# Performance work log

Hardware: AMD Instinct MI355X
Metric: run time of the kernel (lower is better)

The kernel has to match this reference:

```python
import jax, jax.numpy as jnp
import numpy as np

B, S, D, H = 2, 2048, 1024, 16
HD = D // H
SCALE_FACTOR = 0.2  # ScalableSoftmax scale


def setup_inputs() -> dict:
    key = jax.random.key(0)
    ks = jax.random.split(key, 5)
    inv = 1.0 / np.sqrt(D)
    return {
        "x": jax.random.normal(ks[0], (B, S, D), dtype=jnp.float32),
        "qkv_w": jax.random.normal(ks[1], (3 * D, D), dtype=jnp.float32) * inv,
        "qkv_b": jax.random.normal(ks[2], (3 * D,), dtype=jnp.float32) * 0.02,
        "out_w": jax.random.normal(ks[3], (D, D), dtype=jnp.float32) * inv,
        "out_b": jax.random.normal(ks[4], (D,), dtype=jnp.float32) * 0.02,
    }


def reference(x, qkv_w, qkv_b, out_w, out_b):
    b, s, d = x.shape
    # qkv projection: [b, s, 3d] -> [b, h, s, 3*hd]
    qkv = (jnp.einsum("bsd,ed->bse", x, qkv_w) + qkv_b)
    qkv = qkv.reshape(b, s, H, 3 * HD).transpose(0, 2, 1, 3)
    q, k, v = jnp.split(qkv, 3, axis=-1)  # each [b, h, s, hd]
    # scaled dot-product scores, then ScalableSoftmax: softmax(0.2 * scores)
    scores = jnp.einsum("bhqd,bhkd->bhqk", q, k) / jnp.sqrt(jnp.float32(HD))
    attn = jax.nn.softmax(SCALE_FACTOR * scores, axis=-1)
    vals = jnp.einsum("bhqk,bhkd->bhqd", attn, v)
    vals = vals.transpose(0, 2, 1, 3).reshape(b, s, d)
    return jnp.einsum("bsd,ed->bse", vals, out_w) + out_b
```

## Files before the change

### kernel.cpp

```cpp
#include <hip/hip_runtime.h>

using bh8    = __attribute__((ext_vector_type(8)))  short;
using f32x4v = __attribute__((ext_vector_type(4)))  float;
using f32x16 = __attribute__((ext_vector_type(16))) float;
using u32x4  = __attribute__((ext_vector_type(4)))  unsigned int;
using us4    = __attribute__((ext_vector_type(4)))  unsigned short;

#define AS1 __attribute__((address_space(1)))
#define AS3 __attribute__((address_space(3)))

#define B_  2
#define S_  2048
#define D_  1024
#define H_  16
#define HD_ 64
#define C2A 0.0360673760222241f

__device__ __forceinline__ unsigned short f2bf(float f) {
  unsigned u = __builtin_bit_cast(unsigned, f);
  return (unsigned short)((u + 0x7fffu + ((u >> 16) & 1u)) >> 16);
}
__device__ __forceinline__ int swz8(int r) { return (r ^ (r >> 3)) & 7; }

__global__ __launch_bounds__(256) void cvt_all(const float* __restrict__ x,
                                               const float* __restrict__ qw,
                                               const float* __restrict__ ow,
                                               unsigned short* __restrict__ xb,
                                               unsigned short* __restrict__ qwb,
                                               unsigned short* __restrict__ owb) {
  int i = blockIdx.x * 256 + threadIdx.x;
  const float* src; unsigned short* dst; int off;
  if (i < 1048576)      { src = x;  dst = xb;  off = i; }
  else if (i < 1835008) { src = qw; dst = qwb; off = i - 1048576; }
  else                  { src = ow; dst = owb; off = i - 1835008; }
  f32x4v v = reinterpret_cast<const f32x4v*>(src)[off];
  us4 o;
  o[0] = f2bf(v[0]); o[1] = f2bf(v[1]); o[2] = f2bf(v[2]); o[3] = f2bf(v[3]);
  reinterpret_cast<us4*>(dst)[off] = o;
}

template <int MODE, int BM>
__global__ __launch_bounds__(256) void gemm_bt(const unsigned short* __restrict__ A,
                                               const unsigned short* __restrict__ Bw,
                                               const float* __restrict__ bias,
                                               float* __restrict__ Cf,
                                               unsigned short* __restrict__ Qo,
                                               unsigned short* __restrict__ Ko,
                                               unsigned short* __restrict__ Vo,
                                               int M, int N, int K) {
  constexpr int NIW = (BM == 128) ? 4 : 2;
  constexpr int NA  = BM / 32;
  __shared__ __align__(16) short As[BM * 64];
  __shared__ __align__(16) short Bs[128 * 64];
  const int tid = threadIdx.x;
  const int w = tid >> 6, l = tid & 63;
  const int lr = l & 15, lg = l >> 4;
  const int m0 = blockIdx.x * BM, n0 = blockIdx.y * 128;
  const int wm = (BM == 128) ? (w >> 1) * 64 : 0;
  const int wn = (BM == 128) ? (w & 1) * 64 : w * 32;

  f32x4v acc[4][NIW];
#pragma unroll
  for (int a = 0; a < 4; a++)
#pragma unroll
    for (int b = 0; b < NIW; b++)
#pragma unroll
      for (int r = 0; r < 4; r++) acc[a][b][r] = 0.f;

#pragma unroll 1
  for (int k0 = 0; k0 < K; k0 += 64) {
    __syncthreads();
#pragma unroll
    for (int n = 0; n < NA; n++) {
      int idx = n * 256 + tid;
      int row = idx >> 3, p = idx & 7;
      int c = p ^ swz8(row);
      const unsigned short* srcA = A + (size_t)(m0 + row) * K + k0 + c * 8;
      __builtin_amdgcn_global_load_lds((const AS1 void*)srcA,
          (AS3 void*)((char*)As + (n * 256 + w * 64) * 16), 16, 0, 0);
    }
#pragma unroll
    for (int n = 0; n < 4; n++) {
      int idx = n * 256 + tid;
      int row = idx >> 3, p = idx & 7;
      int c = p ^ swz8(row);
      const unsigned short* srcB = Bw + (size_t)(n0 + row) * K + k0 + c * 8;
      __builtin_amdgcn_global_load_lds((const AS1 void*)srcB,
          (AS3 void*)((char*)Bs + (n * 256 + w * 64) * 16), 16, 0, 0);
    }
    __syncthreads();
#pragma unroll
    for (int kk = 0; kk < 2; kk++) {
      bh8 af[4], bf[NIW];
#pragma unroll
      for (int mi = 0; mi < 4; mi++) {
        int row = wm + mi * 16 + lr;
        int slot = (4 * kk + lg) ^ swz8(row);
        af[mi] = *(const bh8*)((const char*)As + row * 128 + slot * 16);
      }
#pragma unroll
      for (int ni = 0; ni < NIW; ni++) {
        int row = wn + ni * 16 + lr;
        int slot = (4 * kk + lg) ^ swz8(row);
        bf[ni] = *(const bh8*)((const char*)Bs + row * 128 + slot * 16);
      }
#pragma unroll
      for (int mi = 0; mi < 4; mi++)
#pragma unroll
        for (int ni = 0; ni < NIW; ni++)
          acc[mi][ni] = __builtin_amdgcn_mfma_f32_16x16x32_bf16(af[mi], bf[ni], acc[mi][ni], 0, 0, 0);
    }
  }

  if (MODE == 1) {
#pragma unroll
    for (int ni = 0; ni < NIW; ni++) {
      int e = n0 + wn + ni * 16 + lr;
      float bv = bias[e];
#pragma unroll
      for (int mi = 0; mi < 4; mi++) {
        int mbase = m0 + wm + mi * 16 + lg * 4;
#pragma unroll
        for (int r = 0; r < 4; r++)
          Cf[(size_t)(mbase + r) * N + e] = acc[mi][ni][r] + bv;
      }
    }
  } else {
#pragma unroll
    for (int ni = 0; ni < NIW; ni++) {
      int e = n0 + wn + ni * 16 + lr;
      int hh = e / 192;
      int rr = e - hh * 192;
      int tsel = rr >> 6, d = rr & 63;
      float bv = bias[e];
#pragma unroll
      for (int mi = 0; mi < 4; mi++) {
        int mbase = m0 + wm + mi * 16 + lg * 4;
#pragma unroll
        for (int r = 0; r < 4; r++) {
          int m = mbase + r;
          int b = m >> 11, s = m & 2047;
          float val = acc[mi][ni][r] + bv;
          size_t bh = (size_t)(b * H_ + hh);
          if (tsel == 0)      Qo[(bh * S_ + s) * HD_ + d] = f2bf(val * C2A);
          else if (tsel == 1) Ko[(bh * S_ + s) * HD_ + d] = f2bf(val);
          else                Vo[(bh * HD_ + d) * S_ + s] = f2bf(val);
        }
      }
    }
  }
}

__global__ __launch_bounds__(512) void attn_fwd(const unsigned short* __restrict__ Qt,
                                                const unsigned short* __restrict__ Kt,
                                                const unsigned short* __restrict__ VT,
                                                unsigned short* __restrict__ vals) {
  __shared__ __align__(16) short Ks[2 * 64 * 64];
  __shared__ __align__(16) short Vs[2 * 64 * 64];
  const int tid = threadIdx.x, w = tid >> 6, l = tid & 63;
  const int lq = l & 31, h = l >> 5;
  const int lin = blockIdx.x;
  const int uu_ = lin >> 3;
  const int bh = (lin & 7) + 8 * (uu_ & 3);
  const int q0 = (uu_ >> 2) * 256 + w * 32;
  const unsigned short* Qp = Qt + (size_t)bh * (S_ * HD_);
  const unsigned short* Kp = Kt + (size_t)bh * (S_ * HD_);
  const unsigned short* Vp = VT + (size_t)bh * (HD_ * S_);

  bh8 qf[4];
#pragma unroll
  for (int kf = 0; kf < 4; kf++)
    qf[kf] = *(const bh8*)(Qp + (size_t)(q0 + lq) * HD_ + kf * 16 + h * 8);

  f32x16 KZ;
#pragma unroll
  for (int r = 0; r < 16; r++) KZ[r] = 0.f;
  bh8 ones;
#pragma unroll
  for (int j = 0; j < 8; j++) ones[j] = (short)0x3F80;

  f32x16 O[2], Ol;
  O[0] = KZ; O[1] = KZ; Ol = KZ;

  const int row0 = tid >> 3, cc = (tid & 7) ^ swz8(row0);
  const unsigned short* kp0 = Kp + row0 * HD_ + cc * 8;
  const unsigned short* vp0 = Vp + (size_t)row0 * S_ + cc * 8;
  char* dK = (char*)Ks + w * 1024;
  char* dV = (char*)Vs + w * 1024;

  auto stage = [&](int t, int buf) {
    __builtin_amdgcn_global_load_lds((const AS1 void*)(kp0 + (size_t)t * 4096),
                                     (AS3 void*)(dK + buf * 8192), 16, 0, 0);
    __builtin_amdgcn_global_load_lds((const AS1 void*)(vp0 + (size_t)t * 64),
                                     (AS3 void*)(dV + buf * 8192), 16, 0, 0);
  };

  int ko0[4], ko1[4], vo0[4], vo1[4];
#pragma unroll
  for (int kf = 0; kf < 4; kf++) {
    int r0 = lq, r1 = 32 + lq;
    ko0[kf] = r0 * 128 + (((2 * kf + h) ^ swz8(r0)) << 4);
    ko1[kf] = r1 * 128 + (((2 * kf + h) ^ swz8(r1)) << 4);
  }
#pragma unroll
  for (int c = 0; c < 2; c++)
#pragma unroll
    for (int ni = 0; ni < 2; ni++) {
      int d = ni * 32 + lq;
      vo0[c * 2 + ni] = d * 128 + (((2 * c + h) ^ swz8(d)) << 4);
      vo1[c * 2 + ni] = d * 128 + (((4 + 2 * c + h) ^ swz8(d)) << 4);
    }

  stage(0, 0);
#pragma unroll 1
  for (int i = 0; i < 32; i++) {
    const int cur = i & 1;
    asm volatile("s_waitcnt vmcnt(0)" ::: "memory");
    __builtin_amdgcn_s_barrier();
    if (i < 31) stage(i + 1, cur ^ 1);
    const char* Kc = (const char*)Ks + cur * 8192;
    const char* Vc = (const char*)Vs + cur * 8192;

    f32x16 sa, sb;
    __builtin_amdgcn_s_setprio(1);
    {
      bh8 k0 = *(const bh8*)(Kc + ko0[0]);
      bh8 k1 = *(const bh8*)(Kc + ko1[0]);
      sa = __builtin_amdgcn_mfma_f32_32x32x16_bf16(k0, qf[0], KZ, 0, 0, 0);
      sb = __builtin_amdgcn_mfma_f32_32x32x16_bf16(k1, qf[0], KZ, 0, 0, 0);
    }
#pragma unroll
    for (int kf = 1; kf < 4; kf++) {
      bh8 k0 = *(const bh8*)(Kc + ko0[kf]);
      bh8 k1 = *(const bh8*)(Kc + ko1[kf]);
      sa = __builtin_amdgcn_mfma_f32_32x32x16_bf16(k0, qf[kf], sa, 0, 0, 0);
      sb = __builtin_amdgcn_mfma_f32_32x32x16_bf16(k1, qf[kf], sb, 0, 0, 0);
    }
    __builtin_amdgcn_s_setprio(0);

    float pa_[16], pb_[16];
#pragma unroll
    for (int r = 0; r < 16; r++)
      asm("v_exp_f32 %0, %1" : "=v"(pa_[r]) : "v"(sa[r]));
    unsigned wa0[4], wa1[4];
#pragma unroll
    for (int g = 0; g < 4; g++) {
      asm("v_cvt_pk_bf16_f32 %0, %1, %2" : "=v"(wa0[g]) : "v"(pa_[4 * g]), "v"(pa_[4 * g + 1]));
      asm("v_cvt_pk_bf16_f32 %0, %1, %2" : "=v"(wa1[g]) : "v"(pa_[4 * g + 2]), "v"(pa_[4 * g + 3]));
    }
#pragma unroll
    for (int r = 0; r < 16; r++)
      asm("v_exp_f32 %0, %1" : "=v"(pb_[r]) : "v"(sb[r]));
    unsigned wb0[4], wb1[4];
#pragma unroll
    for (int g = 0; g < 4; g++) {
      asm("v_cvt_pk_bf16_f32 %0, %1, %2" : "=v"(wb0[g]) : "v"(pb_[4 * g]), "v"(pb_[4 * g + 1]));
      asm("v_cvt_pk_bf16_f32 %0, %1, %2" : "=v"(wb1[g]) : "v"(pb_[4 * g + 2]), "v"(pb_[4 * g + 3]));
    }

    bh8 paf[2], pbf[2];
#pragma unroll
    for (int c = 0; c < 2; c++) {
      unsigned x0 = wa0[2 * c], y0 = wa0[2 * c + 1];
      unsigned x1 = wa1[2 * c], y1 = wa1[2 * c + 1];
      asm("v_permlane32_swap_b32 %0, %1" : "+v"(x0), "+v"(y0));
      asm("v_permlane32_swap_b32 %0, %1" : "+v"(x1), "+v"(y1));
      u32x4 up; up[0] = x0; up[1] = x1; up[2] = y0; up[3] = y1;
      paf[c] = __builtin_bit_cast(bh8, up);
    }
#pragma unroll
    for (int c = 0; c < 2; c++) {
      unsigned x0 = wb0[2 * c], y0 = wb0[2 * c + 1];
      unsigned x1 = wb1[2 * c], y1 = wb1[2 * c + 1];
      asm("v_permlane32_swap_b32 %0, %1" : "+v"(x0), "+v"(y0));
      asm("v_permlane32_swap_b32 %0, %1" : "+v"(x1), "+v"(y1));
      u32x4 up; up[0] = x0; up[1] = x1; up[2] = y0; up[3] = y1;
      pbf[c] = __builtin_bit_cast(bh8, up);
    }

    __builtin_amdgcn_s_setprio(1);
#pragma unroll
    for (int c = 0; c < 2; c++) {
      bh8 vf0 = *(const bh8*)(Vc + vo0[c * 2 + 0]);
      bh8 vf1 = *(const bh8*)(Vc + vo0[c * 2 + 1]);
      O[0] = __builtin_amdgcn_mfma_f32_32x32x16_bf16(paf[c], vf0, O[0], 0, 0, 0);
      O[1] = __builtin_amdgcn_mfma_f32_32x32x16_bf16(paf[c], vf1, O[1], 0, 0, 0);
      Ol   = __builtin_amdgcn_mfma_f32_32x32x16_bf16(paf[c], ones, Ol, 0, 0, 0);
    }
#pragma unroll
    for (int c = 0; c < 2; c++) {
      bh8 vf0 = *(const bh8*)(Vc + vo1[c * 2 + 0]);
      bh8 vf1 = *(const bh8*)(Vc + vo1[c * 2 + 1]);
      O[0] = __builtin_amdgcn_mfma_f32_32x32x16_bf16(pbf[c], vf0, O[0], 0, 0, 0);
      O[1] = __builtin_amdgcn_mfma_f32_32x32x16_bf16(pbf[c], vf1, O[1], 0, 0, 0);
      Ol   = __builtin_amdgcn_mfma_f32_32x32x16_bf16(pbf[c], ones, Ol, 0, 0, 0);
    }
    __builtin_amdgcn_s_setprio(0);
  }

  float rl[16];
#pragma unroll
  for (int r = 0; r < 16; r++) rl[r] = __builtin_amdgcn_rcpf(Ol[r]);

  const int b = bh >> 4, hh = bh & 15;
#pragma unroll
  for (int ni = 0; ni < 2; ni++) {
    int d = ni * 32 + lq;
#pragma unroll
    for (int r = 0; r < 16; r++) {
      float vvv = O[ni][r] * rl[r];
      int qg = q0 + 4 * h + 8 * (r >> 2) + (r & 3);
      vals[((size_t)(b * S_ + qg)) * D_ + hh * HD_ + d] = f2bf(vvv);
    }
  }
}

extern "C" void kernel_launch(void* const* d_in, const int* in_sizes, int n_in,
                              void* d_out, int out_size, void* d_ws, size_t ws_size,
                              hipStream_t stream) {
  const float* x     = (const float*)d_in[0];
  const float* qkv_w = (const float*)d_in[1];
  const float* qkv_b = (const float*)d_in[2];
  const float* out_w = (const float*)d_in[3];
  const float* out_b = (const float*)d_in[4];
  float* out = (float*)d_out;

  unsigned short* xb  = (unsigned short*)d_ws;
  unsigned short* qwb = xb  + (size_t)4096 * 1024;
  unsigned short* owb = qwb + (size_t)3072 * 1024;
  unsigned short* Qb  = owb + (size_t)1024 * 1024;
  unsigned short* Kb  = Qb  + (size_t)32 * 2048 * 64;
  unsigned short* Vb  = Kb  + (size_t)32 * 2048 * 64;
  unsigned short* vb  = Vb  + (size_t)32 * 2048 * 64;

  cvt_all<<<8192, 256, 0, stream>>>(x, qkv_w, out_w, xb, qwb, owb);
  gemm_bt<0, 128><<<dim3(32, 24), 256, 0, stream>>>(xb, qwb, qkv_b, nullptr, Qb, Kb, Vb,
                                                    4096, 3072, 1024);
  attn_fwd<<<256, 512, 0, stream>>>(Qb, Kb, Vb, vb);
  gemm_bt<1, 64><<<dim3(64, 8), 256, 0, stream>>>(vb, owb, out_b, out, nullptr, nullptr, nullptr,
                                                  4096, 1024, 1024);
}
```

Measured before the change: 116.9 us.

## Stage two KV tiles per barrier in attention and swizzle GEMM block order

The attention kernel now loads two 64-key K/V tiles per pipeline stage into doubled LDS buffers. This halves the number of barriers and vmcnt waits across the key loop and processes two tiles between each sync. Both GEMMs also remap block IDs so consecutive blocks are spread across the 8 XCDs for better L2 locality. The cost is more LDS per attention block (64KB) and a deeper unrolled body.

```diff
diff --git a/kernel.cpp b/kernel.cpp
--- a/kernel.cpp
+++ b/kernel.cpp
@@ -39,7 +39,7 @@
   reinterpret_cast<us4*>(dst)[off] = o;
 }
 
-template <int MODE, int BM>
+template <int MODE, int BM, int GX, int NW>
 __global__ __launch_bounds__(256) void gemm_bt(const unsigned short* __restrict__ A,
                                                const unsigned short* __restrict__ Bw,
                                                const float* __restrict__ bias,
@@ -55,7 +55,9 @@
   const int tid = threadIdx.x;
   const int w = tid >> 6, l = tid & 63;
   const int lr = l & 15, lg = l >> 4;
-  const int m0 = blockIdx.x * BM, n0 = blockIdx.y * 128;
+  const int lin = blockIdx.y * GX + blockIdx.x;
+  const int sw  = (lin & 7) * (NW / 8) + (lin >> 3);
+  const int m0 = (sw % GX) * BM, n0 = (sw / GX) * 128;
   const int wm = (BM == 128) ? (w >> 1) * 64 : 0;
   const int wn = (BM == 128) ? (w & 1) * 64 : w * 32;
 
@@ -155,8 +157,8 @@
                                                 const unsigned short* __restrict__ Kt,
                                                 const unsigned short* __restrict__ VT,
                                                 unsigned short* __restrict__ vals) {
-  __shared__ __align__(16) short Ks[2 * 64 * 64];
-  __shared__ __align__(16) short Vs[2 * 64 * 64];
+  __shared__ __align__(16) short Ks[2 * 2 * 64 * 64];
+  __shared__ __align__(16) short Vs[2 * 2 * 64 * 64];
   const int tid = threadIdx.x, w = tid >> 6, l = tid & 63;
   const int lq = l & 31, h = l >> 5;
   const int lin = blockIdx.x;
@@ -188,11 +190,17 @@
   char* dK = (char*)Ks + w * 1024;
   char* dV = (char*)Vs + w * 1024;
 
-  auto stage = [&](int t, int buf) {
-    __builtin_amdgcn_global_load_lds((const AS1 void*)(kp0 + (size_t)t * 4096),
-                                     (AS3 void*)(dK + buf * 8192), 16, 0, 0);
-    __builtin_amdgcn_global_load_lds((const AS1 void*)(vp0 + (size_t)t * 64),
-                                     (AS3 void*)(dV + buf * 8192), 16, 0, 0);
+  auto stage = [&](int i, int buf) {
+    const unsigned short* kB = kp0 + (size_t)i * 8192;
+    const unsigned short* vB = vp0 + (size_t)i * 128;
+    __builtin_amdgcn_global_load_lds((const AS1 void*)kB,
+                                     (AS3 void*)(dK + buf * 16384), 16, 0, 0);
+    __builtin_amdgcn_global_load_lds((const AS1 void*)(kB + 4096),
+                                     (AS3 void*)(dK + buf * 16384 + 8192), 16, 0, 0);
+    __builtin_amdgcn_global_load_lds((const AS1 void*)vB,
+                                     (AS3 void*)(dV + buf * 16384), 16, 0, 0);
+    __builtin_amdgcn_global_load_lds((const AS1 void*)(vB + 64),
+                                     (AS3 void*)(dV + buf * 16384 + 8192), 16, 0, 0);
   };
 
   int ko0[4], ko1[4], vo0[4], vo1[4];
@@ -213,89 +221,92 @@
 
   stage(0, 0);
 #pragma unroll 1
-  for (int i = 0; i < 32; i++) {
+  for (int i = 0; i < 16; i++) {
     const int cur = i & 1;
     asm volatile("s_waitcnt vmcnt(0)" ::: "memory");
     __builtin_amdgcn_s_barrier();
-    if (i < 31) stage(i + 1, cur ^ 1);
-    const char* Kc = (const char*)Ks + cur * 8192;
-    const char* Vc = (const char*)Vs + cur * 8192;
-
-    f32x16 sa, sb;
-    __builtin_amdgcn_s_setprio(1);
-    {
-      bh8 k0 = *(const bh8*)(Kc + ko0[0]);
-      bh8 k1 = *(const bh8*)(Kc + ko1[0]);
-      sa = __builtin_amdgcn_mfma_f32_32x32x16_bf16(k0, qf[0], KZ, 0, 0, 0);
-      sb = __builtin_amdgcn_mfma_f32_32x32x16_bf16(k1, qf[0], KZ, 0, 0, 0);
-    }
-#pragma unroll
-    for (int kf = 1; kf < 4; kf++) {
-      bh8 k0 = *(const bh8*)(Kc + ko0[kf]);
-      bh8 k1 = *(const bh8*)(Kc + ko1[kf]);
-      sa = __builtin_amdgcn_mfma_f32_32x32x16_bf16(k0, qf[kf], sa, 0, 0, 0);
-      sb = __builtin_amdgcn_mfma_f32_32x32x16_bf16(k1, qf[kf], sb, 0, 0, 0);
-    }
-    __builtin_amdgcn_s_setprio(0);
-
-    float pa_[16], pb_[16];
-#pragma unroll
-    for (int r = 0; r < 16; r++)
-      asm("v_exp_f32 %0, %1" : "=v"(pa_[r]) : "v"(sa[r]));
-    unsigned wa0[4], wa1[4];
-#pragma unroll
-    for (int g = 0; g < 4; g++) {
-      asm("v_cvt_pk_bf16_f32 %0, %1, %2" : "=v"(wa0[g]) : "v"(pa_[4 * g]), "v"(pa_[4 * g + 1]));
-      asm("v_cvt_pk_bf16_f32 %0, %1, %2" : "=v"(wa1[g]) : "v"(pa_[4 * g + 2]), "v"(pa_[4 * g + 3]));
-    }
-#pragma unroll
-    for (int r = 0; r < 16; r++)
-      asm("v_exp_f32 %0, %1" : "=v"(pb_[r]) : "v"(sb[r]));
-    unsigned wb0[4], wb1[4];
-#pragma unroll
-    for (int g = 0; g < 4; g++) {
-      asm("v_cvt_pk_bf16_f32 %0, %1, %2" : "=v"(wb0[g]) : "v"(pb_[4 * g]), "v"(pb_[4 * g + 1]));
-      asm("v_cvt_pk_bf16_f32 %0, %1, %2" : "=v"(wb1[g]) : "v"(pb_[4 * g + 2]), "v"(pb_[4 * g + 3]));
-    }
-
-    bh8 paf[2], pbf[2];
-#pragma unroll
-    for (int c = 0; c < 2; c++) {
-      unsigned x0 = wa0[2 * c], y0 = wa0[2 * c + 1];
-      unsigned x1 = wa1[2 * c], y1 = wa1[2 * c + 1];
-      asm("v_permlane32_swap_b32 %0, %1" : "+v"(x0), "+v"(y0));
-      asm("v_permlane32_swap_b32 %0, %1" : "+v"(x1), "+v"(y1));
-      u32x4 up; up[0] = x0; up[1] = x1; up[2] = y0; up[3] = y1;
-      paf[c] = __builtin_bit_cast(bh8, up);
-    }
-#pragma unroll
-    for (int c = 0; c < 2; c++) {
-      unsigned x0 = wb0[2 * c], y0 = wb0[2 * c + 1];
-      unsigned x1 = wb1[2 * c], y1 = wb1[2 * c + 1];
-      asm("v_permlane32_swap_b32 %0, %1" : "+v"(x0), "+v"(y0));
-      asm("v_permlane32_swap_b32 %0, %1" : "+v"(x1), "+v"(y1));
-      u32x4 up; up[0] = x0; up[1] = x1; up[2] = y0; up[3] = y1;
-      pbf[c] = __builtin_bit_cast(bh8, up);
-    }
-
-    __builtin_amdgcn_s_setprio(1);
-#pragma unroll
-    for (int c = 0; c < 2; c++) {
-      bh8 vf0 = *(const bh8*)(Vc + vo0[c * 2 + 0]);
-      bh8 vf1 = *(const bh8*)(Vc + vo0[c * 2 + 1]);
-      O[0] = __builtin_amdgcn_mfma_f32_32x32x16_bf16(paf[c], vf0, O[0], 0, 0, 0);
-      O[1] = __builtin_amdgcn_mfma_f32_32x32x16_bf16(paf[c], vf1, O[1], 0, 0, 0);
-      Ol   = __builtin_amdgcn_mfma_f32_32x32x16_bf16(paf[c], ones, Ol, 0, 0, 0);
-    }
-#pragma unroll
-    for (int c = 0; c < 2; c++) {
-      bh8 vf0 = *(const bh8*)(Vc + vo1[c * 2 + 0]);
-      bh8 vf1 = *(const bh8*)(Vc + vo1[c * 2 + 1]);
-      O[0] = __builtin_amdgcn_mfma_f32_32x32x16_bf16(pbf[c], vf0, O[0], 0, 0, 0);
-      O[1] = __builtin_amdgcn_mfma_f32_32x32x16_bf16(pbf[c], vf1, O[1], 0, 0, 0);
-      Ol   = __builtin_amdgcn_mfma_f32_32x32x16_bf16(pbf[c], ones, Ol, 0, 0, 0);
-    }
-    __builtin_amdgcn_s_setprio(0);
+    if (i < 15) stage(i + 1, cur ^ 1);
+#pragma unroll
+    for (int tt = 0; tt < 2; tt++) {
+      const char* Kc = (const char*)Ks + cur * 16384 + tt * 8192;
+      const char* Vc = (const char*)Vs + cur * 16384 + tt * 8192;
+
+      f32x16 sa, sb;
+      __builtin_amdgcn_s_setprio(1);
+      {
+        bh8 k0 = *(const bh8*)(Kc + ko0[0]);
+        bh8 k1 = *(const bh8*)(Kc + ko1[0]);
+        sa = __builtin_amdgcn_mfma_f32_32x32x16_bf16(k0, qf[0], KZ, 0, 0, 0);
+        sb = __builtin_amdgcn_mfma_f32_32x32x16_bf16(k1, qf[0], KZ, 0, 0, 0);
+      }
+#pragma unroll
+      for (int kf = 1; kf < 4; kf++) {
+        bh8 k0 = *(const bh8*)(Kc + ko0[kf]);
+        bh8 k1 = *(const bh8*)(Kc + ko1[kf]);
+        sa = __builtin_amdgcn_mfma_f32_32x32x16_bf16(k0, qf[kf], sa, 0, 0, 0);
+        sb = __builtin_amdgcn_mfma_f32_32x32x16_bf16(k1, qf[kf], sb, 0, 0, 0);
+      }
+      __builtin_amdgcn_s_setprio(0);
+
+      float pa_[16], pb_[16];
+#pragma unroll
+      for (int r = 0; r < 16; r++)
+        asm("v_exp_f32 %0, %1" : "=v"(pa_[r]) : "v"(sa[r]));
+      unsigned wa0[4], wa1[4];
+#pragma unroll
+      for (int g = 0; g < 4; g++) {
+        asm("v_cvt_pk_bf16_f32 %0, %1, %2" : "=v"(wa0[g]) : "v"(pa_[4 * g]), "v"(pa_[4 * g + 1]));
+        asm("v_cvt_pk_bf16_f32 %0, %1, %2" : "=v"(wa1[g]) : "v"(pa_[4 * g + 2]), "v"(pa_[4 * g + 3]));
+      }
+#pragma unroll
+      for (int r = 0; r < 16; r++)
+        asm("v_exp_f32 %0, %1" : "=v"(pb_[r]) : "v"(sb[r]));
+      unsigned wb0[4], wb1[4];
+#pragma unroll
+      for (int g = 0; g < 4; g++) {
+        asm("v_cvt_pk_bf16_f32 %0, %1, %2" : "=v"(wb0[g]) : "v"(pb_[4 * g]), "v"(pb_[4 * g + 1]));
+        asm("v_cvt_pk_bf16_f32 %0, %1, %2" : "=v"(wb1[g]) : "v"(pb_[4 * g + 2]), "v"(pb_[4 * g + 3]));
+      }
+
+      bh8 paf[2], pbf[2];
+#pragma unroll
+      for (int c = 0; c < 2; c++) {
+        unsigned x0 = wa0[2 * c], y0 = wa0[2 * c + 1];
+        unsigned x1 = wa1[2 * c], y1 = wa1[2 * c + 1];
+        asm("v_permlane32_swap_b32 %0, %1" : "+v"(x0), "+v"(y0));
+        asm("v_permlane32_swap_b32 %0, %1" : "+v"(x1), "+v"(y1));
+        u32x4 up; up[0] = x0; up[1] = x1; up[2] = y0; up[3] = y1;
+        paf[c] = __builtin_bit_cast(bh8, up);
+      }
+#pragma unroll
+      for (int c = 0; c < 2; c++) {
+        unsigned x0 = wb0[2 * c], y0 = wb0[2 * c + 1];
+        unsigned x1 = wb1[2 * c], y1 = wb1[2 * c + 1];
+        asm("v_permlane32_swap_b32 %0, %1" : "+v"(x0), "+v"(y0));
+        asm("v_permlane32_swap_b32 %0, %1" : "+v"(x1), "+v"(y1));
+        u32x4 up; up[0] = x0; up[1] = x1; up[2] = y0; up[3] = y1;
+        pbf[c] = __builtin_bit_cast(bh8, up);
+      }
+
+      __builtin_amdgcn_s_setprio(1);
+#pragma unroll
+      for (int c = 0; c < 2; c++) {
+        bh8 vf0 = *(const bh8*)(Vc + vo0[c * 2 + 0]);
+        bh8 vf1 = *(const bh8*)(Vc + vo0[c * 2 + 1]);
+        O[0] = __builtin_amdgcn_mfma_f32_32x32x16_bf16(paf[c], vf0, O[0], 0, 0, 0);
+        O[1] = __builtin_amdgcn_mfma_f32_32x32x16_bf16(paf[c], vf1, O[1], 0, 0, 0);
+        Ol   = __builtin_amdgcn_mfma_f32_32x32x16_bf16(paf[c], ones, Ol, 0, 0, 0);
+      }
+#pragma unroll
+      for (int c = 0; c < 2; c++) {
+        bh8 vf0 = *(const bh8*)(Vc + vo1[c * 2 + 0]);
+        bh8 vf1 = *(const bh8*)(Vc + vo1[c * 2 + 1]);
+        O[0] = __builtin_amdgcn_mfma_f32_32x32x16_bf16(pbf[c], vf0, O[0], 0, 0, 0);
+        O[1] = __builtin_amdgcn_mfma_f32_32x32x16_bf16(pbf[c], vf1, O[1], 0, 0, 0);
+        Ol   = __builtin_amdgcn_mfma_f32_32x32x16_bf16(pbf[c], ones, Ol, 0, 0, 0);
+      }
+      __builtin_amdgcn_s_setprio(0);
+    }
   }
 
   float rl[16];
@@ -334,9 +345,9 @@
   unsigned short* vb  = Vb  + (size_t)32 * 2048 * 64;
 
   cvt_all<<<8192, 256, 0, stream>>>(x, qkv_w, out_w, xb, qwb, owb);
-  gemm_bt<0, 128><<<dim3(32, 24), 256, 0, stream>>>(xb, qwb, qkv_b, nullptr, Qb, Kb, Vb,
-                                                    4096, 3072, 1024);
+  gemm_bt<0, 128, 32, 768><<<dim3(32, 24), 256, 0, stream>>>(xb, qwb, qkv_b, nullptr, Qb, Kb, Vb,
+                                                             4096, 3072, 1024);
   attn_fwd<<<256, 512, 0, stream>>>(Qb, Kb, Vb, vb);
-  gemm_bt<1, 64><<<dim3(64, 8), 256, 0, stream>>>(vb, owb, out_b, out, nullptr, nullptr, nullptr,
-                                                  4096, 1024, 1024);
-}
+  gemm_bt<1, 64, 64, 512><<<dim3(64, 8), 256, 0, stream>>>(vb, owb, out_b, out, nullptr, nullptr, nullptr,
+                                                           4096, 1024, 1024);
+}
```

Measured after the change: 107.2 us. 1.09x faster.
